# Performance work log

Hardware: AMD Instinct MI355X
Metric: run time of the kernel (lower is better)

## Reference

```python
import jax, jax.numpy as jnp
import numpy as np

C = 1.0          # ball curvature (k = -1/c with c=1.0 in the torch module)
SQC = 1.0        # sqrt(C)
LN_EPS = 1e-5

def _artanh(x):
    return jnp.arctanh(jnp.clip(x, -1.0 + 1e-7, 1.0 - 1e-7))

def _norm(x):
    # last-dim L2 norm, clamped away from zero for stable division
    return jnp.clip(jnp.sqrt(jnp.sum(x * x, axis=-1, keepdims=True)), 1e-7, None)

def expmap0(u):
    un = _norm(u)
    return jnp.tanh(SQC * un) * u / (SQC * un)

def logmap0(y):
    yn = _norm(y)
    return _artanh(SQC * yn) * y / (SQC * yn)

def mobius_add(x, y):
    x2 = jnp.sum(x * x, axis=-1, keepdims=True)
    y2 = jnp.sum(y * y, axis=-1, keepdims=True)
    xy = jnp.sum(x * y, axis=-1, keepdims=True)
    num = (1.0 + 2.0 * C * xy + C * y2) * x + (1.0 - C * x2) * y
    den = 1.0 + 2.0 * C * xy + C * C * x2 * y2
    return num / jnp.clip(den, 1e-15, None)

def mobius_matvec(W, x):
    # W: [H, D], x: [B, D] -> [B, H]
    mx = x @ W.T
    xn = _norm(x)
    mxn = _norm(mx)
    res = jnp.tanh(mxn / xn * _artanh(SQC * xn)) * mx / (SQC * mxn)
    return jnp.where(mxn <= 1e-7, jnp.zeros_like(res), res)

def mobius_pointwise_mul(w, x):
    wx = w * x
    xn = _norm(x)
    wxn = _norm(wx)
    res = jnp.tanh(wxn / xn * _artanh(SQC * xn)) * wx / (SQC * wxn)
    return jnp.where(wxn <= 1e-7, jnp.zeros_like(res), res)

def layer_norm(x, g, b):
    mu = jnp.mean(x, axis=-1, keepdims=True)
    var = jnp.mean((x - mu) ** 2, axis=-1, keepdims=True)
    return (x - mu) * jax.lax.rsqrt(var + LN_EPS) * g + b

def one_rnn_transform(W, h, U, x, b):
    Wh = mobius_matvec(W, h)
    Ux = mobius_matvec(U, x)
    return mobius_add(mobius_add(Wh, Ux), b)

def setup_inputs() -> dict:
    key = jax.random.key(0)
    B, I, H = 65536, 256, 256
    k1, k2, k3, k4, k5 = jax.random.split(key, 5)
    stdv = 1.0 / np.sqrt(H)
    # points on the Poincare ball via expmap0 of small tangent vectors
    x = expmap0(0.02 * jax.random.normal(k1, (B, I), dtype=jnp.float32))
    hx = expmap0(0.02 * jax.random.normal(k2, (B, H), dtype=jnp.float32))
    weight_ih = jax.random.uniform(k3, (3 * H, I), dtype=jnp.float32, minval=-stdv, maxval=stdv)
    weight_hh = jax.random.uniform(k4, (3 * H, H), dtype=jnp.float32, minval=-stdv, maxval=stdv)
    bias = 0.01 * jax.random.normal(k5, (3, H), dtype=jnp.float32)
    ln_gamma = jnp.ones((3, H), dtype=jnp.float32)
    ln_beta = jnp.zeros((3, H), dtype=jnp.float32)
    return {"input": x, "hx": hx, "weight_ih": weight_ih, "weight_hh": weight_hh,
            "bias": bias, "ln_gamma": ln_gamma, "ln_beta": ln_beta}

def reference(input, hx, weight_ih, weight_hh, bias, ln_gamma, ln_beta):
    H = hx.shape[-1]
    W_ir, W_ih_, W_iz = weight_ih[:H], weight_ih[H:2*H], weight_ih[2*H:]
    W_hr, W_hh_, W_hz = weight_hh[:H], weight_hh[H:2*H], weight_hh[2*H:]
    b_r, b_h, b_z = bias[0], bias[1], bias[2]
    temp_z = logmap0(one_rnn_transform(W_hz, hx, W_iz, input, b_z))
    temp_r = logmap0(one_rnn_transform(W_hr, hx, W_ir, input, b_r))
    z_t = jax.nn.sigmoid(layer_norm(temp_z, ln_gamma[0], ln_beta[0]))
    r_t = jax.nn.sigmoid(layer_norm(temp_r, ln_gamma[1], ln_beta[1]))
    rh_t = mobius_pointwise_mul(r_t, hx)
    h_tilde = one_rnn_transform(W_hh_, rh_t, W_ih_, input, b_h)
    h_tilde = expmap0(jnp.tanh(layer_norm(logmap0(h_tilde), ln_gamma[2], ln_beta[2])))
    temp_1 = mobius_pointwise_mul(1.0 - z_t, hx)
    temp_2 = mobius_pointwise_mul(z_t, h_tilde)
    return mobius_add(temp_1, temp_2)
```

## Files before the change

kernel.cpp:

```cpp
#include <hip/hip_runtime.h>
#include <math.h>

#define HD  256
#define BM  16
#define NTH 256

typedef __attribute__((ext_vector_type(8))) short bf16x8;
typedef __attribute__((ext_vector_type(4))) float f32x4;

__device__ __forceinline__ float rcp_f(float x){ return __builtin_amdgcn_rcpf(x); }
__device__ __forceinline__ float tanh_f(float x){
  float ax = fabsf(x);
  float e  = __expf(-2.f*ax);
  float t  = (1.f - e) * rcp_f(1.f + e);
  return copysignf(t, x);
}
__device__ __forceinline__ float artanh_f(float v){
  v = fminf(fmaxf(v, -1.f + 1e-7f), 1.f - 1e-7f);
  return 0.5f * __logf((1.f + v) * rcp_f(1.f - v));
}
__device__ __forceinline__ float sigmoid_f(float v){ return rcp_f(1.f + __expf(-v)); }
__device__ __forceinline__ unsigned short f2bf(float f){
  unsigned u = __float_as_uint(f);
  u += 0x7FFFu + ((u >> 16) & 1u);
  return (unsigned short)(u >> 16);
}
__device__ __forceinline__ float bf2f(unsigned short h){
  return __uint_as_float(((unsigned)h) << 16);
}
__device__ __forceinline__ int swz(int R, int C){
  return R*HD + (((C >> 3) ^ (R & 7)) << 3) + (C & 7);
}

__global__ void convert_w_kernel(const float* __restrict__ Wih,
                                 const float* __restrict__ Whh,
                                 unsigned short* __restrict__ wb){
  int c = blockIdx.x * blockDim.x + threadIdx.x;
  if (c >= 6 * 8192) return;
  int mat = c >> 13;
  int ci  = c & 8191;
  int l = ci & 63, st = ci >> 6;
  int s = st & 7, ct = st >> 3;
  int col = ct * 16 + (l & 15);
  int k0  = s * 32 + (l >> 4) * 8;
  const float* src = (mat < 3) ? (Wih + (size_t)mat * HD * HD)
                               : (Whh + (size_t)(mat - 3) * HD * HD);
  const float* p = src + (size_t)col * HD + k0;
  unsigned short tmp[8];
  #pragma unroll
  for (int j = 0; j < 8; ++j) tmp[j] = f2bf(p[j]);
  *(bf16x8*)(wb + (size_t)mat * 65536 + (size_t)ci * 8) = *(bf16x8*)tmp;
}

__device__ __forceinline__ void gate_gemm(
    const unsigned short* ldsH, const unsigned short* __restrict__ wH,
    const unsigned short* ldsX, const unsigned short* __restrict__ wX,
    f32x4 A[4], f32x4 Bx[4], int wc, int lr, int lg, int l){
  #pragma unroll
  for (int n = 0; n < 4; ++n){
    A[n]  = (f32x4){0.f,0.f,0.f,0.f};
    Bx[n] = (f32x4){0.f,0.f,0.f,0.f};
  }
  #pragma unroll
  for (int s = 0; s < 8; ++s){
    int idx = lr*HD + (((4*s + lg) ^ (lr & 7)) << 3);
    bf16x8 ah = *(const bf16x8*)&ldsH[idx];
    bf16x8 ax = *(const bf16x8*)&ldsX[idx];
    #pragma unroll
    for (int n = 0; n < 4; ++n){
      int ct = wc*4 + n;
      int off = ((ct*8 + s)*64 + l)*8;
      bf16x8 bh = *(const bf16x8*)(wH + off);
      bf16x8 bx = *(const bf16x8*)(wX + off);
      A[n]  = __builtin_amdgcn_mfma_f32_16x16x32_bf16(ah, bh, A[n], 0, 0, 0);
      Bx[n] = __builtin_amdgcn_mfma_f32_16x16x32_bf16(ax, bx, Bx[n], 0, 0, 0);
    }
  }
}

__device__ __forceinline__ void gate_reduce_chain(
    const f32x4 (&A)[4], const f32x4 (&Bx)[4], const float (&bt)[4],
    float (*RED)[33], float (*kco)[9], float (*srow)[BM], const float* sbb,
    int rowA, int gidx, int t, int wc, int lr, int lg){
  float p[7][4];
  #pragma unroll
  for (int q = 0; q < 4; ++q){
    float a2=0.f,b2=0.f,ab=0.f,sA=0.f,sB=0.f,Ab=0.f,Bb=0.f;
    #pragma unroll
    for (int n = 0; n < 4; ++n){
      float ae = A[n][q], be = Bx[n][q], bv = bt[n];
      a2 = fmaf(ae,ae,a2); b2 = fmaf(be,be,b2); ab = fmaf(ae,be,ab);
      sA += ae; sB += be; Ab = fmaf(ae,bv,Ab); Bb = fmaf(be,bv,Bb);
    }
    p[0][q]=a2; p[1][q]=b2; p[2][q]=ab; p[3][q]=sA; p[4][q]=sB; p[5][q]=Ab; p[6][q]=Bb;
  }
  #pragma unroll
  for (int j = 0; j < 7; ++j)
    #pragma unroll
    for (int q = 0; q < 4; ++q){
      float v = p[j][q];
      v += __shfl_xor(v,1); v += __shfl_xor(v,2);
      v += __shfl_xor(v,4); v += __shfl_xor(v,8);
      p[j][q] = v;
    }
  if (lr == 0){
    #pragma unroll
    for (int q = 0; q < 4; ++q){
      int R = lg*4 + q;
      #pragma unroll
      for (int j = 0; j < 7; ++j) RED[R][wc*8 + j] = p[j][q];
    }
  }
  __syncthreads();
  if (t < BM){
    int R = t;
    float s[7];
    #pragma unroll
    for (int j = 0; j < 7; ++j)
      s[j] = RED[R][j] + RED[R][8+j] + RED[R][16+j] + RED[R][24+j];
    float bb  = sbb[gidx];
    float sbs = sbb[4+gidx];
    float an = srow[rowA][R], aa = srow[rowA+1][R];
    float bn = srow[0][R],    ba = srow[1][R];
    float mraw = sqrtf(s[0]); float mA = fmaxf(mraw, 1e-7f);
    float tA = tanh_f(mA / an * aa);
    float sa  = (mraw <= 1e-7f) ? 0.f : tA / mA;
    float x2a = (mraw <= 1e-7f) ? 0.f : tA*tA;
    float nraw = sqrtf(s[1]); float mB = fmaxf(nraw, 1e-7f);
    float tB = tanh_f(mB / bn * ba);
    float sb_ = (nraw <= 1e-7f) ? 0.f : tB / mB;
    float x2b = (nraw <= 1e-7f) ? 0.f : tB*tB;
    float xy = sa*sb_*s[2];
    float ca = 1.f + 2.f*xy + x2b;
    float cb = 1.f - x2a;
    float den = fmaxf(1.f + 2.f*xy + x2a*x2b, 1e-15f);
    float u = ca*sa/den, v = cb*sb_/den;
    float P2 = u*u*s[0] + 2.f*u*v*s[2] + v*v*s[1];
    float Pb = u*s[5] + v*s[6];
    float sP = u*s[3] + v*s[4];
    float ca2 = 1.f + 2.f*Pb + bb;
    float cb2 = 1.f - P2;
    float den2 = fmaxf(1.f + 2.f*Pb + P2*bb, 1e-15f);
    float pp = ca2/den2, ww = cb2/den2;
    float Q2 = pp*pp*P2 + 2.f*pp*ww*Pb + ww*ww*bb;
    float sQsum = pp*sP + ww*sbs;
    float qn = fmaxf(sqrtf(Q2), 1e-7f);
    float sQ = artanh_f(qn) / qn;
    float mu = sQ*sQsum*(1.f/HD);
    float e2 = sQ*sQ*Q2*(1.f/HD);
    float is = rsqrtf(e2 - mu*mu + 1e-5f);
    kco[R][0] = sQ*pp*u;  kco[R][1] = sQ*pp*v;  kco[R][2] = sQ*ww;
    kco[R][3] = mu;       kco[R][4] = is;
  }
  __syncthreads();
}

__global__ __launch_bounds__(NTH, 2) void mobius_gru_mfma(
    const float* __restrict__ x, const float* __restrict__ hx,
    const unsigned short* __restrict__ wbih, const unsigned short* __restrict__ wbhh,
    const float* __restrict__ bias, const float* __restrict__ gam,
    const float* __restrict__ bet, float* __restrict__ out, int B){
  __shared__ unsigned short xb[BM*HD];
  __shared__ unsigned short hb[BM*HD];
  __shared__ float RED[BM][33];
  __shared__ float kco[BM][9];
  __shared__ float srow[8][BM];
  __shared__ float sbb[8];

  const int t  = threadIdx.x;
  const int l  = t & 63;
  const int lr = l & 15, lg = l >> 4;
  const int wc = t >> 6;
  const size_t row0 = (size_t)blockIdx.x * BM;

  {
    float* spart = &RED[0][0];
    int r = t >> 4, seg = t & 15;
    const float* xp = x  + (row0 + r)*HD + seg*16;
    const float* hp = hx + (row0 + r)*HD + seg*16;
    float sx = 0.f, sh = 0.f;
    #pragma unroll
    for (int i = 0; i < 4; ++i){
      int c = seg*16 + i*4;
      int di = swz(r, c);
      float4 v = *(const float4*)(xp + i*4);
      sx += v.x*v.x + v.y*v.y + v.z*v.z + v.w*v.w;
      ushort4 o = { f2bf(v.x), f2bf(v.y), f2bf(v.z), f2bf(v.w) };
      *(ushort4*)&xb[di] = o;
      v = *(const float4*)(hp + i*4);
      sh += v.x*v.x + v.y*v.y + v.z*v.z + v.w*v.w;
      ushort4 o2 = { f2bf(v.x), f2bf(v.y), f2bf(v.z), f2bf(v.w) };
      *(ushort4*)&hb[di] = o2;
    }
    spart[r*16 + seg] = sx; spart[256 + r*16 + seg] = sh;
  }
  if (t >= 64 && t < 256){
    int g = (t >> 6) - 1;
    float4 b4 = *(const float4*)&bias[g*HD + (t & 63)*4];
    float p2 = b4.x*b4.x + b4.y*b4.y + b4.z*b4.z + b4.w*b4.w;
    float ps = b4.x + b4.y + b4.z + b4.w;
    #pragma unroll
    for (int m = 1; m <= 32; m <<= 1){ p2 += __shfl_xor(p2, m); ps += __shfl_xor(ps, m); }
    if ((t & 63) == 0){ sbb[g] = p2; sbb[4+g] = ps; }
  }
  __syncthreads();
  if (t < BM){
    float* spart = &RED[0][0];
    float sx = 0.f, sh = 0.f;
    #pragma unroll
    for (int i = 0; i < 16; ++i){ sx += spart[t*16 + i]; sh += spart[256 + t*16 + i]; }
    float xn = fmaxf(sqrtf(sx), 1e-7f);
    float hn = fmaxf(sqrtf(sh), 1e-7f);
    srow[0][t] = xn; srow[1][t] = artanh_f(xn);
    srow[2][t] = hn; srow[3][t] = artanh_f(hn);
  }
  __syncthreads();

  f32x4 A[4], Bx[4];
  float bt[4], gv[4], bv[4];
  unsigned ztp[4][2];
  float hvreg[4][4];

  #pragma unroll
  for (int n = 0; n < 4; ++n){
    int C = wc*64 + n*16 + lr;
    bt[n] = bias[2*HD + C]; gv[n] = gam[C]; bv[n] = bet[C];
  }
  gate_gemm(hb, wbhh + 2*65536, xb, wbih + 2*65536, A, Bx, wc, lr, lg, l);
  gate_reduce_chain(A, Bx, bt, RED, kco, srow, sbb, 2, 2, t, wc, lr, lg);
  #pragma unroll
  for (int q = 0; q < 4; ++q){
    int R = lg*4 + q;
    float KA=kco[R][0], KB=kco[R][1], Kb=kco[R][2], mu=kco[R][3], is=kco[R][4];
    #pragma unroll
    for (int n = 0; n < 4; ++n){
      float ln = (KA*A[n][q] + KB*Bx[n][q] + Kb*bt[n] - mu)*is*gv[n] + bv[n];
      unsigned zb = f2bf(sigmoid_f(ln));
      if ((q & 1) == 0) ztp[n][q>>1] = zb;
      else              ztp[n][q>>1] |= (zb << 16);
    }
  }

  #pragma unroll
  for (int n = 0; n < 4; ++n){
    int C = wc*64 + n*16 + lr;
    bt[n] = bias[C]; gv[n] = gam[HD + C]; bv[n] = bet[HD + C];
  }
  gate_gemm(hb, wbhh, xb, wbih, A, Bx, wc, lr, lg, l);
  gate_reduce_chain(A, Bx, bt, RED, kco, srow, sbb, 2, 0, t, wc, lr, lg);
  {
    #pragma unroll
    for (int q = 0; q < 4; ++q){
      int R = lg*4 + q;
      float KA=kco[R][0], KB=kco[R][1], Kb=kco[R][2], mu=kco[R][3], is=kco[R][4];
      float acc = 0.f;
      #pragma unroll
      for (int n = 0; n < 4; ++n){
        int C = wc*64 + n*16 + lr;
        float hv = bf2f(hb[swz(R, C)]);
        hvreg[n][q] = hv;
        float ln = (KA*A[n][q] + KB*Bx[n][q] + Kb*bt[n] - mu)*is*gv[n] + bv[n];
        float rhv = sigmoid_f(ln) * hv;
        Bx[n][q] = rhv;
        acc = fmaf(rhv, rhv, acc);
      }
      float v2 = acc;
      v2 += __shfl_xor(v2,1); v2 += __shfl_xor(v2,2);
      v2 += __shfl_xor(v2,4); v2 += __shfl_xor(v2,8);
      if (lr == 0) RED[R][wc*8] = v2;
    }
  }
  __syncthreads();
  if (t < BM){
    int R = t;
    float s0 = RED[R][0] + RED[R][8] + RED[R][16] + RED[R][24];
    float wraw = sqrtf(s0); float wn = fmaxf(wraw, 1e-7f);
    float s = tanh_f(wn / srow[2][R] * srow[3][R]);
    float sc = (wraw <= 1e-7f) ? 0.f : s / wn;
    float rn = fmaxf((wraw <= 1e-7f) ? 0.f : fabsf(s), 1e-7f);
    kco[R][0] = sc; srow[4][R] = rn; srow[5][R] = artanh_f(rn);
  }
  __syncthreads();
  #pragma unroll
  for (int q = 0; q < 4; ++q){
    int R = lg*4 + q;
    float sc = kco[R][0];
    #pragma unroll
    for (int n = 0; n < 4; ++n){
      int C = wc*64 + n*16 + lr;
      hb[swz(R, C)] = f2bf(sc * Bx[n][q]);
    }
  }
  __syncthreads();

  #pragma unroll
  for (int n = 0; n < 4; ++n){
    int C = wc*64 + n*16 + lr;
    bt[n] = bias[HD + C]; gv[n] = gam[2*HD + C]; bv[n] = bet[2*HD + C];
  }
  gate_gemm(hb, wbhh + 65536, xb, wbih + 65536, A, Bx, wc, lr, lg, l);
  gate_reduce_chain(A, Bx, bt, RED, kco, srow, sbb, 4, 1, t, wc, lr, lg);
  {
    #pragma unroll
    for (int q = 0; q < 4; ++q){
      int R = lg*4 + q;
      float KA=kco[R][0], KB=kco[R][1], Kb=kco[R][2], mu=kco[R][3], is=kco[R][4];
      float acc = 0.f;
      #pragma unroll
      for (int n = 0; n < 4; ++n){
        float ln = (KA*A[n][q] + KB*Bx[n][q] + Kb*bt[n] - mu)*is*gv[n] + bv[n];
        float uv = tanh_f(ln);
        A[n][q] = uv;
        acc = fmaf(uv, uv, acc);
      }
      float v2 = acc;
      v2 += __shfl_xor(v2,1); v2 += __shfl_xor(v2,2);
      v2 += __shfl_xor(v2,4); v2 += __shfl_xor(v2,8);
      if (lr == 0) RED[R][wc*8] = v2;
    }
  }
  __syncthreads();
  if (t < BM){
    int R = t;
    float s0 = RED[R][0] + RED[R][8] + RED[R][16] + RED[R][24];
    float unraw = sqrtf(s0);
    float un = fmaxf(unraw, 1e-7f);
    float es = tanh_f(un) / un;
    float htn = fmaxf(es * unraw, 1e-7f);
    kco[R][0] = es; srow[6][R] = htn; srow[7][R] = artanh_f(htn);
  }
  __syncthreads();

  #pragma unroll
  for (int q = 0; q < 4; ++q){
    int R = lg*4 + q;
    float es = kco[R][0];
    float a1 = 0.f, a2 = 0.f, a12 = 0.f;
    #pragma unroll
    for (int n = 0; n < 4; ++n){
      unsigned zp = ztp[n][q >> 1];
      float zv = __uint_as_float((q & 1) ? (zp & 0xFFFF0000u) : (zp << 16));
      float w2v = zv * es * A[n][q];
      float w1v = (1.f - zv) * hvreg[n][q];
      A[n][q]  = w1v;
      Bx[n][q] = w2v;
      a1 = fmaf(w1v, w1v, a1); a2 = fmaf(w2v, w2v, a2); a12 = fmaf(w1v, w2v, a12);
    }
    float v1 = a1, v2 = a2, v3 = a12;
    v1 += __shfl_xor(v1,1); v2 += __shfl_xor(v2,1); v3 += __shfl_xor(v3,1);
    v1 += __shfl_xor(v1,2); v2 += __shfl_xor(v2,2); v3 += __shfl_xor(v3,2);
    v1 += __shfl_xor(v1,4); v2 += __shfl_xor(v2,4); v3 += __shfl_xor(v3,4);
    v1 += __shfl_xor(v1,8); v2 += __shfl_xor(v2,8); v3 += __shfl_xor(v3,8);
    if (lr == 0){
      RED[R][wc*8]   = v1;
      RED[R][wc*8+1] = v2;
      RED[R][wc*8+2] = v3;
    }
  }
  __syncthreads();
  if (t < BM){
    int R = t;
    float s1  = RED[R][0] + RED[R][8]  + RED[R][16] + RED[R][24];
    float s2  = RED[R][1] + RED[R][9]  + RED[R][17] + RED[R][25];
    float s12 = RED[R][2] + RED[R][10] + RED[R][18] + RED[R][26];
    float raw1 = sqrtf(s1); float n1 = fmaxf(raw1, 1e-7f);
    float ss1 = tanh_f(n1 / srow[2][R] * srow[3][R]);
    float sc1 = (raw1 <= 1e-7f) ? 0.f : ss1 / n1;
    float t1  = (raw1 <= 1e-7f) ? 0.f : ss1*ss1;
    float raw2 = sqrtf(s2); float n2 = fmaxf(raw2, 1e-7f);
    float ss2 = tanh_f(n2 / srow[6][R] * srow[7][R]);
    float sc2 = (raw2 <= 1e-7f) ? 0.f : ss2 / n2;
    float t2  = (raw2 <= 1e-7f) ? 0.f : ss2*ss2;
    float xy = sc1*sc2*s12;
    float ca = 1.f + 2.f*xy + t2;
    float cb = 1.f - t1;
    float den = fmaxf(1.f + 2.f*xy + t1*t2, 1e-15f);
    kco[R][0] = ca*sc1/den;
    kco[R][1] = cb*sc2/den;
  }
  __syncthreads();
  #pragma unroll
  for (int q = 0; q < 4; ++q){
    int R = lg*4 + q;
    float cw1 = kco[R][0], cw2 = kco[R][1];
    #pragma unroll
    for (int n = 0; n < 4; ++n){
      int C = wc*64 + n*16 + lr;
      out[(row0 + R)*HD + C] = cw1*A[n][q] + cw2*Bx[n][q];
    }
  }
}

extern "C" void kernel_launch(void* const* d_in, const int* in_sizes, int n_in,
                              void* d_out, int out_size, void* d_ws, size_t ws_size,
                              hipStream_t stream){
  const float* x    = (const float*)d_in[0];
  const float* hx   = (const float*)d_in[1];
  const float* Wih  = (const float*)d_in[2];
  const float* Whh  = (const float*)d_in[3];
  const float* bias = (const float*)d_in[4];
  const float* gam  = (const float*)d_in[5];
  const float* bet  = (const float*)d_in[6];
  float* out = (float*)d_out;
  unsigned short* wb = (unsigned short*)d_ws;
  const int B = in_sizes[0] / HD;

  hipLaunchKernelGGL(convert_w_kernel, dim3(192), dim3(256), 0, stream, Wih, Whh, wb);
  hipLaunchKernelGGL(mobius_gru_mfma, dim3(B / BM), dim3(NTH), 0, stream,
                     x, hx, wb, wb + 3*65536, bias, gam, bet, out, B);
}
```

Measured before the change: 222.8 us.

## Use two waves per block with 8 column tiles each and fewer barriers

Halves the block to 128 threads (2 waves), so each wave now computes 128 output columns with 8 MFMA accumulator tiles per gate instead of 4. Cross-wave reductions drop from 4 partials to 2. Some per-row scalar steps now run redundantly in every wave through shuffles, which removes several __syncthreads. The reset-scaled hidden state goes into a separate LDS buffer with the scale folded into the accumulators after the GEMM, and hx values are re-read from LDS rather than held in registers. In exchange, register pressure per thread rises and there are fewer waves per CU to hide latency.

```diff
diff --git a/kernel.cpp b/kernel.cpp
--- a/kernel.cpp
+++ b/kernel.cpp
@@ -3,7 +3,7 @@
 
 #define HD  256
 #define BM  16
-#define NTH 256
+#define NTH 128
 
 typedef __attribute__((ext_vector_type(8))) short bf16x8;
 typedef __attribute__((ext_vector_type(4))) float f32x4;
@@ -52,43 +52,42 @@
   *(bf16x8*)(wb + (size_t)mat * 65536 + (size_t)ci * 8) = *(bf16x8*)tmp;
 }
 
-__device__ __forceinline__ void gate_gemm(
-    const unsigned short* ldsH, const unsigned short* __restrict__ wH,
-    const unsigned short* ldsX, const unsigned short* __restrict__ wX,
-    f32x4 A[4], f32x4 Bx[4], int wc, int lr, int lg, int l){
-  #pragma unroll
-  for (int n = 0; n < 4; ++n){
+__device__ __forceinline__ void gate_gemm8(
+    const unsigned short* ldsA, const unsigned short* __restrict__ wA,
+    const unsigned short* ldsB, const unsigned short* __restrict__ wB,
+    f32x4 A[8], f32x4 Bx[8], int wc, int lr, int lg, int l){
+  #pragma unroll
+  for (int n = 0; n < 8; ++n){
     A[n]  = (f32x4){0.f,0.f,0.f,0.f};
     Bx[n] = (f32x4){0.f,0.f,0.f,0.f};
   }
   #pragma unroll
   for (int s = 0; s < 8; ++s){
     int idx = lr*HD + (((4*s + lg) ^ (lr & 7)) << 3);
-    bf16x8 ah = *(const bf16x8*)&ldsH[idx];
-    bf16x8 ax = *(const bf16x8*)&ldsX[idx];
-    #pragma unroll
-    for (int n = 0; n < 4; ++n){
-      int ct = wc*4 + n;
+    bf16x8 fa = *(const bf16x8*)&ldsA[idx];
+    bf16x8 fb = *(const bf16x8*)&ldsB[idx];
+    #pragma unroll
+    for (int n = 0; n < 8; ++n){
+      int ct = wc*8 + n;
       int off = ((ct*8 + s)*64 + l)*8;
-      bf16x8 bh = *(const bf16x8*)(wH + off);
-      bf16x8 bx = *(const bf16x8*)(wX + off);
-      A[n]  = __builtin_amdgcn_mfma_f32_16x16x32_bf16(ah, bh, A[n], 0, 0, 0);
-      Bx[n] = __builtin_amdgcn_mfma_f32_16x16x32_bf16(ax, bx, Bx[n], 0, 0, 0);
-    }
-  }
-}
-
-__device__ __forceinline__ void gate_reduce_chain(
-    const f32x4 (&A)[4], const f32x4 (&Bx)[4], const float (&bt)[4],
-    float (*RED)[33], float (*kco)[9], float (*srow)[BM], const float* sbb,
-    int rowA, int gidx, int t, int wc, int lr, int lg){
+      bf16x8 wa = *(const bf16x8*)(wA + off);
+      bf16x8 wb_ = *(const bf16x8*)(wB + off);
+      A[n]  = __builtin_amdgcn_mfma_f32_16x16x32_bf16(fa, wa, A[n], 0, 0, 0);
+      Bx[n] = __builtin_amdgcn_mfma_f32_16x16x32_bf16(fb, wb_, Bx[n], 0, 0, 0);
+    }
+  }
+}
+
+__device__ __forceinline__ void reduce7(
+    const f32x4* A, const f32x4* B, const float* bt,
+    float (*RED)[17], int wc, int lr, int lg){
   float p[7][4];
   #pragma unroll
   for (int q = 0; q < 4; ++q){
     float a2=0.f,b2=0.f,ab=0.f,sA=0.f,sB=0.f,Ab=0.f,Bb=0.f;
     #pragma unroll
-    for (int n = 0; n < 4; ++n){
-      float ae = A[n][q], be = Bx[n][q], bv = bt[n];
+    for (int n = 0; n < 8; ++n){
+      float ae = A[n][q], be = B[n][q], bv = bt[n];
       a2 = fmaf(ae,ae,a2); b2 = fmaf(be,be,b2); ab = fmaf(ae,be,ab);
       sA += ae; sB += be; Ab = fmaf(ae,bv,Ab); Bb = fmaf(be,bv,Bb);
     }
@@ -111,48 +110,40 @@
       for (int j = 0; j < 7; ++j) RED[R][wc*8 + j] = p[j][q];
     }
   }
-  __syncthreads();
-  if (t < BM){
-    int R = t;
-    float s[7];
-    #pragma unroll
-    for (int j = 0; j < 7; ++j)
-      s[j] = RED[R][j] + RED[R][8+j] + RED[R][16+j] + RED[R][24+j];
-    float bb  = sbb[gidx];
-    float sbs = sbb[4+gidx];
-    float an = srow[rowA][R], aa = srow[rowA+1][R];
-    float bn = srow[0][R],    ba = srow[1][R];
-    float mraw = sqrtf(s[0]); float mA = fmaxf(mraw, 1e-7f);
-    float tA = tanh_f(mA / an * aa);
-    float sa  = (mraw <= 1e-7f) ? 0.f : tA / mA;
-    float x2a = (mraw <= 1e-7f) ? 0.f : tA*tA;
-    float nraw = sqrtf(s[1]); float mB = fmaxf(nraw, 1e-7f);
-    float tB = tanh_f(mB / bn * ba);
-    float sb_ = (nraw <= 1e-7f) ? 0.f : tB / mB;
-    float x2b = (nraw <= 1e-7f) ? 0.f : tB*tB;
-    float xy = sa*sb_*s[2];
-    float ca = 1.f + 2.f*xy + x2b;
-    float cb = 1.f - x2a;
-    float den = fmaxf(1.f + 2.f*xy + x2a*x2b, 1e-15f);
-    float u = ca*sa/den, v = cb*sb_/den;
-    float P2 = u*u*s[0] + 2.f*u*v*s[2] + v*v*s[1];
-    float Pb = u*s[5] + v*s[6];
-    float sP = u*s[3] + v*s[4];
-    float ca2 = 1.f + 2.f*Pb + bb;
-    float cb2 = 1.f - P2;
-    float den2 = fmaxf(1.f + 2.f*Pb + P2*bb, 1e-15f);
-    float pp = ca2/den2, ww = cb2/den2;
-    float Q2 = pp*pp*P2 + 2.f*pp*ww*Pb + ww*ww*bb;
-    float sQsum = pp*sP + ww*sbs;
-    float qn = fmaxf(sqrtf(Q2), 1e-7f);
-    float sQ = artanh_f(qn) / qn;
-    float mu = sQ*sQsum*(1.f/HD);
-    float e2 = sQ*sQ*Q2*(1.f/HD);
-    float is = rsqrtf(e2 - mu*mu + 1e-5f);
-    kco[R][0] = sQ*pp*u;  kco[R][1] = sQ*pp*v;  kco[R][2] = sQ*ww;
-    kco[R][3] = mu;       kco[R][4] = is;
-  }
-  __syncthreads();
+}
+
+__device__ __forceinline__ void chain5(
+    const float* s, float bb, float sbs,
+    float an, float aa, float bn, float ba, float* o){
+  float mraw = sqrtf(s[0]); float mA = fmaxf(mraw, 1e-7f);
+  float tA = tanh_f(mA / an * aa);
+  float sa  = (mraw <= 1e-7f) ? 0.f : tA / mA;
+  float x2a = (mraw <= 1e-7f) ? 0.f : tA*tA;
+  float nraw = sqrtf(s[1]); float mB = fmaxf(nraw, 1e-7f);
+  float tB = tanh_f(mB / bn * ba);
+  float sb_ = (nraw <= 1e-7f) ? 0.f : tB / mB;
+  float x2b = (nraw <= 1e-7f) ? 0.f : tB*tB;
+  float xy = sa*sb_*s[2];
+  float ca = 1.f + 2.f*xy + x2b;
+  float cb = 1.f - x2a;
+  float den = fmaxf(1.f + 2.f*xy + x2a*x2b, 1e-15f);
+  float u = ca*sa/den, v = cb*sb_/den;
+  float P2 = u*u*s[0] + 2.f*u*v*s[2] + v*v*s[1];
+  float Pb = u*s[5] + v*s[6];
+  float sP = u*s[3] + v*s[4];
+  float ca2 = 1.f + 2.f*Pb + bb;
+  float cb2 = 1.f - P2;
+  float den2 = fmaxf(1.f + 2.f*Pb + P2*bb, 1e-15f);
+  float pp = ca2/den2, ww = cb2/den2;
+  float Q2 = pp*pp*P2 + 2.f*pp*ww*Pb + ww*ww*bb;
+  float sQsum = pp*sP + ww*sbs;
+  float qn = fmaxf(sqrtf(Q2), 1e-7f);
+  float sQ = artanh_f(qn) / qn;
+  float mu = sQ*sQsum*(1.f/HD);
+  float e2 = sQ*sQ*Q2*(1.f/HD);
+  float is = rsqrtf(e2 - mu*mu + 1e-5f);
+  o[0] = sQ*pp*u;  o[1] = sQ*pp*v;  o[2] = sQ*ww;
+  o[3] = mu;       o[4] = is;
 }
 
 __global__ __launch_bounds__(NTH, 2) void mobius_gru_mfma(
@@ -162,8 +153,10 @@
     const float* __restrict__ bet, float* __restrict__ out, int B){
   __shared__ unsigned short xb[BM*HD];
   __shared__ unsigned short hb[BM*HD];
-  __shared__ float RED[BM][33];
-  __shared__ float kco[BM][9];
+  __shared__ unsigned short rhb[BM*HD];
+  __shared__ float RED[BM][17];
+  __shared__ float spart[2*NTH];
+  __shared__ float kco[BM][10];
   __shared__ float srow[8][BM];
   __shared__ float sbb[8];
 
@@ -174,14 +167,13 @@
   const size_t row0 = (size_t)blockIdx.x * BM;
 
   {
-    float* spart = &RED[0][0];
-    int r = t >> 4, seg = t & 15;
-    const float* xp = x  + (row0 + r)*HD + seg*16;
-    const float* hp = hx + (row0 + r)*HD + seg*16;
+    int r = t >> 3, seg = t & 7;
+    const float* xp = x  + (row0 + r)*HD + seg*32;
+    const float* hp = hx + (row0 + r)*HD + seg*32;
     float sx = 0.f, sh = 0.f;
     #pragma unroll
-    for (int i = 0; i < 4; ++i){
-      int c = seg*16 + i*4;
+    for (int i = 0; i < 8; ++i){
+      int c = seg*32 + i*4;
       int di = swz(r, c);
       float4 v = *(const float4*)(xp + i*4);
       sx += v.x*v.x + v.y*v.y + v.z*v.z + v.w*v.w;
@@ -192,122 +184,160 @@
       ushort4 o2 = { f2bf(v.x), f2bf(v.y), f2bf(v.z), f2bf(v.w) };
       *(ushort4*)&hb[di] = o2;
     }
-    spart[r*16 + seg] = sx; spart[256 + r*16 + seg] = sh;
-  }
-  if (t >= 64 && t < 256){
-    int g = (t >> 6) - 1;
-    float4 b4 = *(const float4*)&bias[g*HD + (t & 63)*4];
+    spart[t] = sx; spart[NTH + t] = sh;
+  }
+  for (int g = wc; g < 3; g += 2){
+    float4 b4 = *(const float4*)&bias[g*HD + l*4];
     float p2 = b4.x*b4.x + b4.y*b4.y + b4.z*b4.z + b4.w*b4.w;
     float ps = b4.x + b4.y + b4.z + b4.w;
     #pragma unroll
     for (int m = 1; m <= 32; m <<= 1){ p2 += __shfl_xor(p2, m); ps += __shfl_xor(ps, m); }
-    if ((t & 63) == 0){ sbb[g] = p2; sbb[4+g] = ps; }
-  }
+    if (l == 0){ sbb[g] = p2; sbb[4+g] = ps; }
+  }
+  __syncthreads();
+  if (t < 32){
+    int R = t & 15, sel = t >> 4;
+    const float* base = spart + sel*NTH;
+    float sv = 0.f;
+    #pragma unroll
+    for (int i = 0; i < 8; ++i) sv += base[R*8 + i];
+    float nn = fmaxf(sqrtf(sv), 1e-7f);
+    srow[sel*2][R] = nn; srow[sel*2+1][R] = artanh_f(nn);
+  }
+  __syncthreads();
+
+  f32x4 A[8], Bx[8];
+  float bt[8];
+  unsigned ztp[8][2];
+
+  #pragma unroll
+  for (int n = 0; n < 8; ++n) bt[n] = bias[2*HD + wc*128 + n*16 + lr];
+  gate_gemm8(hb, wbhh + 2*65536, xb, wbih + 2*65536, A, Bx, wc, lr, lg, l);
+  reduce7(A, Bx, bt, RED, wc, lr, lg);
   __syncthreads();
   if (t < BM){
-    float* spart = &RED[0][0];
-    float sx = 0.f, sh = 0.f;
-    #pragma unroll
-    for (int i = 0; i < 16; ++i){ sx += spart[t*16 + i]; sh += spart[256 + t*16 + i]; }
-    float xn = fmaxf(sqrtf(sx), 1e-7f);
-    float hn = fmaxf(sqrtf(sh), 1e-7f);
-    srow[0][t] = xn; srow[1][t] = artanh_f(xn);
-    srow[2][t] = hn; srow[3][t] = artanh_f(hn);
-  }
-  __syncthreads();
-
-  f32x4 A[4], Bx[4];
-  float bt[4], gv[4], bv[4];
-  unsigned ztp[4][2];
-  float hvreg[4][4];
-
-  #pragma unroll
-  for (int n = 0; n < 4; ++n){
-    int C = wc*64 + n*16 + lr;
-    bt[n] = bias[2*HD + C]; gv[n] = gam[C]; bv[n] = bet[C];
-  }
-  gate_gemm(hb, wbhh + 2*65536, xb, wbih + 2*65536, A, Bx, wc, lr, lg, l);
-  gate_reduce_chain(A, Bx, bt, RED, kco, srow, sbb, 2, 2, t, wc, lr, lg);
-  #pragma unroll
-  for (int q = 0; q < 4; ++q){
-    int R = lg*4 + q;
-    float KA=kco[R][0], KB=kco[R][1], Kb=kco[R][2], mu=kco[R][3], is=kco[R][4];
-    #pragma unroll
-    for (int n = 0; n < 4; ++n){
-      float ln = (KA*A[n][q] + KB*Bx[n][q] + Kb*bt[n] - mu)*is*gv[n] + bv[n];
-      unsigned zb = f2bf(sigmoid_f(ln));
-      if ((q & 1) == 0) ztp[n][q>>1] = zb;
-      else              ztp[n][q>>1] |= (zb << 16);
-    }
-  }
-
-  #pragma unroll
-  for (int n = 0; n < 4; ++n){
-    int C = wc*64 + n*16 + lr;
-    bt[n] = bias[C]; gv[n] = gam[HD + C]; bv[n] = bet[HD + C];
-  }
-  gate_gemm(hb, wbhh, xb, wbih, A, Bx, wc, lr, lg, l);
-  gate_reduce_chain(A, Bx, bt, RED, kco, srow, sbb, 2, 0, t, wc, lr, lg);
-  {
+    int R = t;
+    float s[7];
+    #pragma unroll
+    for (int j = 0; j < 7; ++j) s[j] = RED[R][j] + RED[R][8+j];
+    float o[5];
+    chain5(s, sbb[2], sbb[6], srow[2][R], srow[3][R], srow[0][R], srow[1][R], o);
+    #pragma unroll
+    for (int k = 0; k < 5; ++k) kco[R][k] = o[k];
+  }
+  __syncthreads();
+  {
+    float gv[8], bv[8];
+    #pragma unroll
+    for (int n = 0; n < 8; ++n){
+      int C = wc*128 + n*16 + lr;
+      gv[n] = gam[C]; bv[n] = bet[C];
+    }
+    #pragma unroll
+    for (int q = 0; q < 4; ++q){
+      int R = lg*4 + q;
+      float KA=kco[R][0], KB=kco[R][1], Kb=kco[R][2], mu=kco[R][3], is=kco[R][4];
+      #pragma unroll
+      for (int n = 0; n < 8; ++n){
+        float ln = (KA*A[n][q] + KB*Bx[n][q] + Kb*bt[n] - mu)*is*gv[n] + bv[n];
+        unsigned zb = f2bf(sigmoid_f(ln));
+        if ((q & 1) == 0) ztp[n][q>>1] = zb;
+        else              ztp[n][q>>1] |= (zb << 16);
+      }
+    }
+  }
+
+  #pragma unroll
+  for (int n = 0; n < 8; ++n) bt[n] = bias[wc*128 + n*16 + lr];
+  gate_gemm8(hb, wbhh, xb, wbih, A, Bx, wc, lr, lg, l);
+  reduce7(A, Bx, bt, RED, wc, lr, lg);
+  __syncthreads();
+  if (t < BM){
+    int R = t;
+    float s[7];
+    #pragma unroll
+    for (int j = 0; j < 7; ++j) s[j] = RED[R][j] + RED[R][8+j];
+    float o[5];
+    chain5(s, sbb[0], sbb[4], srow[2][R], srow[3][R], srow[0][R], srow[1][R], o);
+    #pragma unroll
+    for (int k = 0; k < 5; ++k) kco[R][k] = o[k];
+  }
+  __syncthreads();
+  {
+    float gv[8], bv[8];
+    #pragma unroll
+    for (int n = 0; n < 8; ++n){
+      int C = wc*128 + n*16 + lr;
+      gv[n] = gam[HD + C]; bv[n] = bet[HD + C];
+    }
     #pragma unroll
     for (int q = 0; q < 4; ++q){
       int R = lg*4 + q;
       float KA=kco[R][0], KB=kco[R][1], Kb=kco[R][2], mu=kco[R][3], is=kco[R][4];
       float acc = 0.f;
       #pragma unroll
-      for (int n = 0; n < 4; ++n){
-        int C = wc*64 + n*16 + lr;
+      for (int n = 0; n < 8; ++n){
+        int C = wc*128 + n*16 + lr;
         float hv = bf2f(hb[swz(R, C)]);
-        hvreg[n][q] = hv;
         float ln = (KA*A[n][q] + KB*Bx[n][q] + Kb*bt[n] - mu)*is*gv[n] + bv[n];
         float rhv = sigmoid_f(ln) * hv;
-        Bx[n][q] = rhv;
+        rhb[swz(R, C)] = f2bf(rhv);
         acc = fmaf(rhv, rhv, acc);
       }
       float v2 = acc;
       v2 += __shfl_xor(v2,1); v2 += __shfl_xor(v2,2);
       v2 += __shfl_xor(v2,4); v2 += __shfl_xor(v2,8);
-      if (lr == 0) RED[R][wc*8] = v2;
-    }
-  }
+      if (lr == 0) RED[R][wc*8 + 7] = v2;
+    }
+  }
+  __syncthreads();
+  float scq[4];
+  {
+    int crow = lg*4 + (lr & 3);
+    float s0 = RED[crow][7] + RED[crow][15];
+    float wraw = sqrtf(s0); float wn = fmaxf(wraw, 1e-7f);
+    float sv = tanh_f(wn / srow[2][crow] * srow[3][crow]);
+    float sc = (wraw <= 1e-7f) ? 0.f : sv / wn;
+    float rn = fmaxf((wraw <= 1e-7f) ? 0.f : fabsf(sv), 1e-7f);
+    if (wc == 0 && lr < 4){ srow[4][crow] = rn; srow[5][crow] = artanh_f(rn); }
+    #pragma unroll
+    for (int q = 0; q < 4; ++q) scq[q] = __shfl(sc, (l & 48) + q);
+  }
+
+  #pragma unroll
+  for (int n = 0; n < 8; ++n) bt[n] = bias[HD + wc*128 + n*16 + lr];
+  gate_gemm8(rhb, wbhh + 65536, xb, wbih + 65536, A, Bx, wc, lr, lg, l);
+  #pragma unroll
+  for (int n = 0; n < 8; ++n)
+    #pragma unroll
+    for (int q = 0; q < 4; ++q) A[n][q] *= scq[q];
+  reduce7(A, Bx, bt, RED, wc, lr, lg);
   __syncthreads();
   if (t < BM){
     int R = t;
-    float s0 = RED[R][0] + RED[R][8] + RED[R][16] + RED[R][24];
-    float wraw = sqrtf(s0); float wn = fmaxf(wraw, 1e-7f);
-    float s = tanh_f(wn / srow[2][R] * srow[3][R]);
-    float sc = (wraw <= 1e-7f) ? 0.f : s / wn;
-    float rn = fmaxf((wraw <= 1e-7f) ? 0.f : fabsf(s), 1e-7f);
-    kco[R][0] = sc; srow[4][R] = rn; srow[5][R] = artanh_f(rn);
-  }
-  __syncthreads();
-  #pragma unroll
-  for (int q = 0; q < 4; ++q){
-    int R = lg*4 + q;
-    float sc = kco[R][0];
-    #pragma unroll
-    for (int n = 0; n < 4; ++n){
-      int C = wc*64 + n*16 + lr;
-      hb[swz(R, C)] = f2bf(sc * Bx[n][q]);
-    }
-  }
-  __syncthreads();
-
-  #pragma unroll
-  for (int n = 0; n < 4; ++n){
-    int C = wc*64 + n*16 + lr;
-    bt[n] = bias[HD + C]; gv[n] = gam[2*HD + C]; bv[n] = bet[2*HD + C];
-  }
-  gate_gemm(hb, wbhh + 65536, xb, wbih + 65536, A, Bx, wc, lr, lg, l);
-  gate_reduce_chain(A, Bx, bt, RED, kco, srow, sbb, 4, 1, t, wc, lr, lg);
-  {
+    float s[7];
+    #pragma unroll
+    for (int j = 0; j < 7; ++j) s[j] = RED[R][j] + RED[R][8+j];
+    float o[5];
+    chain5(s, sbb[1], sbb[5], srow[4][R], srow[5][R], srow[0][R], srow[1][R], o);
+    #pragma unroll
+    for (int k = 0; k < 5; ++k) kco[R][k] = o[k];
+  }
+  __syncthreads();
+  {
+    float gv[8], bv[8];
+    #pragma unroll
+    for (int n = 0; n < 8; ++n){
+      int C = wc*128 + n*16 + lr;
+      gv[n] = gam[2*HD + C]; bv[n] = bet[2*HD + C];
+    }
     #pragma unroll
     for (int q = 0; q < 4; ++q){
       int R = lg*4 + q;
       float KA=kco[R][0], KB=kco[R][1], Kb=kco[R][2], mu=kco[R][3], is=kco[R][4];
       float acc = 0.f;
       #pragma unroll
-      for (int n = 0; n < 4; ++n){
+      for (int n = 0; n < 8; ++n){
         float ln = (KA*A[n][q] + KB*Bx[n][q] + Kb*bt[n] - mu)*is*gv[n] + bv[n];
         float uv = tanh_f(ln);
         A[n][q] = uv;
@@ -316,34 +346,37 @@
       float v2 = acc;
       v2 += __shfl_xor(v2,1); v2 += __shfl_xor(v2,2);
       v2 += __shfl_xor(v2,4); v2 += __shfl_xor(v2,8);
-      if (lr == 0) RED[R][wc*8] = v2;
-    }
-  }
-  __syncthreads();
-  if (t < BM){
-    int R = t;
-    float s0 = RED[R][0] + RED[R][8] + RED[R][16] + RED[R][24];
+      if (lr == 0) RED[R][wc*8 + 7] = v2;
+    }
+  }
+  __syncthreads();
+  float esq[4];
+  {
+    int crow = lg*4 + (lr & 3);
+    float s0 = RED[crow][7] + RED[crow][15];
     float unraw = sqrtf(s0);
     float un = fmaxf(unraw, 1e-7f);
     float es = tanh_f(un) / un;
     float htn = fmaxf(es * unraw, 1e-7f);
-    kco[R][0] = es; srow[6][R] = htn; srow[7][R] = artanh_f(htn);
-  }
-  __syncthreads();
+    if (wc == 0 && lr < 4){ srow[6][crow] = htn; srow[7][crow] = artanh_f(htn); }
+    #pragma unroll
+    for (int q = 0; q < 4; ++q) esq[q] = __shfl(es, (l & 48) + q);
+  }
 
   #pragma unroll
   for (int q = 0; q < 4; ++q){
     int R = lg*4 + q;
-    float es = kco[R][0];
     float a1 = 0.f, a2 = 0.f, a12 = 0.f;
     #pragma unroll
-    for (int n = 0; n < 4; ++n){
+    for (int n = 0; n < 8; ++n){
+      int C = wc*128 + n*16 + lr;
       unsigned zp = ztp[n][q >> 1];
       float zv = __uint_as_float((q & 1) ? (zp & 0xFFFF0000u) : (zp << 16));
-      float w2v = zv * es * A[n][q];
-      float w1v = (1.f - zv) * hvreg[n][q];
-      A[n][q]  = w1v;
-      Bx[n][q] = w2v;
+      float hv = bf2f(hb[swz(R, C)]);
+      float w2v = zv * esq[q] * A[n][q];
+      float w1v = (1.f - zv) * hv;
+      A[n][q]  = w2v;
+      Bx[n][q] = w1v;
       a1 = fmaf(w1v, w1v, a1); a2 = fmaf(w2v, w2v, a2); a12 = fmaf(w1v, w2v, a12);
     }
     float v1 = a1, v2 = a2, v3 = a12;
@@ -360,9 +393,9 @@
   __syncthreads();
   if (t < BM){
     int R = t;
-    float s1  = RED[R][0] + RED[R][8]  + RED[R][16] + RED[R][24];
-    float s2  = RED[R][1] + RED[R][9]  + RED[R][17] + RED[R][25];
-    float s12 = RED[R][2] + RED[R][10] + RED[R][18] + RED[R][26];
+    float s1  = RED[R][0] + RED[R][8];
+    float s2  = RED[R][1] + RED[R][9];
+    float s12 = RED[R][2] + RED[R][10];
     float raw1 = sqrtf(s1); float n1 = fmaxf(raw1, 1e-7f);
     float ss1 = tanh_f(n1 / srow[2][R] * srow[3][R]);
     float sc1 = (raw1 <= 1e-7f) ? 0.f : ss1 / n1;
@@ -384,9 +417,9 @@
     int R = lg*4 + q;
     float cw1 = kco[R][0], cw2 = kco[R][1];
     #pragma unroll
-    for (int n = 0; n < 4; ++n){
-      int C = wc*64 + n*16 + lr;
-      out[(row0 + R)*HD + C] = cw1*A[n][q] + cw2*Bx[n][q];
+    for (int n = 0; n < 8; ++n){
+      int C = wc*128 + n*16 + lr;
+      out[(row0 + R)*HD + C] = cw1*Bx[n][q] + cw2*A[n][q];
     }
   }
 }
```

New measurement: 337.1 us. +51.3%, slower.
